# Kernel tuning notes

Hardware: AMD Instinct MI355X
Metric: run time of the kernel (lower is better)

## Reference

```python
import jax, jax.numpy as jnp
import numpy as np

N_USERS = 200000
N_ITEMS = 100000
LATENT_DIM = 32
N_INTER = 1000000  # user-item interactions; symmetric adjacency has 2*N_INTER edges


def setup_inputs() -> dict:
    key = jax.random.key(0)
    ku, ki = jax.random.split(key)
    user_emb = jax.random.normal(ku, (N_USERS, LATENT_DIM), dtype=jnp.float32) * 0.1
    item_emb = jax.random.normal(ki, (N_ITEMS, LATENT_DIM), dtype=jnp.float32) * 0.1

    # Build the symmetric normalized adjacency L = D^-0.5 A D^-0.5 in COO form,
    # mirroring get_norm_adj_mat(). Users occupy rows [0, n_users), items rows
    # [n_users, n_users+n_items).
    rng = np.random.default_rng(0)
    u = rng.integers(0, N_USERS, size=N_INTER).astype(np.int32)
    it = rng.integers(0, N_ITEMS, size=N_INTER).astype(np.int32) + N_USERS
    row = np.concatenate([u, it])   # [2*N_INTER]
    col = np.concatenate([it, u])   # [2*N_INTER]
    deg = np.bincount(row, minlength=N_USERS + N_ITEMS).astype(np.float32)
    dinv = np.power(deg + 1e-7, -0.5).astype(np.float32)
    val = dinv[row] * dinv[col]

    return {
        "user_emb": user_emb,
        "item_emb": item_emb,
        "adj_row": jnp.asarray(row, dtype=jnp.int32),
        "adj_col": jnp.asarray(col, dtype=jnp.int32),
        "adj_val": jnp.asarray(val, dtype=jnp.float32),
        "n_layers": 3,
    }


def reference(user_emb, item_emb, adj_row, adj_col, adj_val, n_layers):
    n_users = user_emb.shape[0]
    n_nodes = n_users + item_emb.shape[0]
    e = jnp.concatenate([user_emb, item_emb], axis=0)  # [N, D] ego embeddings
    acc = e
    for _ in range(n_layers):
        # SpMM: e <- L @ e via gather + segment_sum over COO edges
        msgs = adj_val[:, None] * e[adj_col]               # [nnz, D]
        e = jax.ops.segment_sum(msgs, adj_row, num_segments=n_nodes)
        acc = acc + e
    out = acc / float(n_layers + 1)  # mean over stacked layer embeddings
    return out[:n_users], out[n_users:]
```

## Files before the change

### kernel.cpp

```cpp
#include <hip/hip_runtime.h>

#define D 32
#define BSH 9
#define BRWS 512
#define EC 8192
#define NBMAX 1024

__device__ __forceinline__ unsigned short f2bf(float f) {
    unsigned u = __float_as_uint(f);
    return (unsigned short)((u + 0x7FFFu + ((u >> 16) & 1u)) >> 16);
}
__device__ __forceinline__ float bflo(unsigned v) { return __uint_as_float(v << 16); }
__device__ __forceinline__ float bfhi(unsigned v) { return __uint_as_float(v & 0xFFFF0000u); }

__global__ void zero_int_kernel(int* __restrict__ p, int n) {
    int i = blockIdx.x * blockDim.x + threadIdx.x;
    if (i < n) p[i] = 0;
}

__global__ void bhist_kernel(const int* __restrict__ row, int* __restrict__ gcnt,
                             int nnz, int nb) {
    __shared__ int h[NBMAX];
    for (int i = threadIdx.x; i < NBMAX; i += blockDim.x) h[i] = 0;
    __syncthreads();
    int stride = gridDim.x * blockDim.x;
    for (int i = blockIdx.x * blockDim.x + threadIdx.x; i < nnz; i += stride)
        atomicAdd(&h[row[i] >> BSH], 1);
    __syncthreads();
    for (int i = threadIdx.x; i < nb; i += blockDim.x)
        if (h[i]) atomicAdd(&gcnt[i], h[i]);
}

__global__ void bscan_kernel(const int* __restrict__ gcnt, int* __restrict__ gbase,
                             int* __restrict__ gcur, int nb, int nnz) {
    __shared__ int lds[256];
    int t = threadIdx.x;
    int base = t * 4;
    int v[4];
    int s = 0;
#pragma unroll
    for (int k = 0; k < 4; ++k) {
        v[k] = (base + k < nb) ? gcnt[base + k] : 0;
        s += v[k];
    }
    lds[t] = s;
    __syncthreads();
    for (int off = 1; off < 256; off <<= 1) {
        int x = lds[t];
        int y = (t >= off) ? lds[t - off] : 0;
        __syncthreads();
        lds[t] = x + y;
        __syncthreads();
    }
    int run = lds[t] - s;
#pragma unroll
    for (int k = 0; k < 4; ++k) {
        if (base + k < nb) { gbase[base + k] = run; gcur[base + k] = run; }
        run += v[k];
    }
    if (t == 0) gbase[nb] = nnz;
}

__global__ __launch_bounds__(256) void part_kernel(
    const int* __restrict__ row, const int* __restrict__ col,
    int* __restrict__ gcur, unsigned* __restrict__ be, int nnz) {
    __shared__ int h[NBMAX];
    __shared__ int cur[NBMAX];
    int c0 = blockIdx.x * EC;
    int c1 = c0 + EC;
    if (c1 > nnz) c1 = nnz;
    for (int i = threadIdx.x; i < NBMAX; i += blockDim.x) h[i] = 0;
    __syncthreads();
    for (int i = c0 + threadIdx.x; i < c1; i += blockDim.x)
        atomicAdd(&h[row[i] >> BSH], 1);
    __syncthreads();
    for (int i = threadIdx.x; i < NBMAX; i += blockDim.x) {
        int c = h[i];
        cur[i] = c ? atomicAdd(&gcur[i], c) : 0;
    }
    __syncthreads();
    for (int i = c0 + threadIdx.x; i < c1; i += blockDim.x) {
        int r = row[i];
        int pos = atomicAdd(&cur[r >> BSH], 1);
        be[pos] = ((unsigned)(r & (BRWS - 1)) << 19) | (unsigned)col[i];
    }
}

__global__ __launch_bounds__(256) void lcsr_kernel(
    const int* __restrict__ gbase, const unsigned* __restrict__ be,
    int* __restrict__ ci, int* __restrict__ ptr,
    float* __restrict__ dinv, float* __restrict__ rds,
    int n_nodes, int nnz) {
    __shared__ int cnt[BRWS];
    __shared__ int cur[BRWS];
    __shared__ int sc[256];
    int b = blockIdx.x;
    int t = threadIdx.x;
    cnt[2 * t] = 0;
    cnt[2 * t + 1] = 0;
    __syncthreads();
    int s0 = gbase[b], s1 = gbase[b + 1];
    for (int j = s0 + t; j < s1; j += 256)
        atomicAdd(&cnt[be[j] >> 19], 1);
    __syncthreads();
    int v0 = cnt[2 * t], v1 = cnt[2 * t + 1];
    int s = v0 + v1;
    sc[t] = s;
    __syncthreads();
    for (int off = 1; off < 256; off <<= 1) {
        int x = sc[t];
        int y = (t >= off) ? sc[t - off] : 0;
        __syncthreads();
        sc[t] = x + y;
        __syncthreads();
    }
    int ex = sc[t] - s;
    int gr = b * BRWS + 2 * t;
    if (gr < n_nodes) {
        ptr[gr] = s0 + ex;
        float r_ = sqrtf((float)v0 + 1e-7f);
        dinv[gr] = 1.0f / r_;
        rds[gr] = r_;
    }
    if (gr + 1 < n_nodes) {
        ptr[gr + 1] = s0 + ex + v0;
        float r_ = sqrtf((float)v1 + 1e-7f);
        dinv[gr + 1] = 1.0f / r_;
        rds[gr + 1] = r_;
    }
    cur[2 * t] = s0 + ex;
    cur[2 * t + 1] = s0 + ex + v0;
    if (b == 0 && t == 0) ptr[n_nodes] = nnz;
    __syncthreads();
    for (int j = s0 + t; j < s1; j += 256) {
        unsigned e = be[j];
        int pos = atomicAdd(&cur[e >> 19], 1);
        ci[pos] = (int)((e & 0x7FFFFu) << 5);
    }
}

__global__ void init_em_kernel(const float* __restrict__ ue, const float* __restrict__ ie,
                               const float* __restrict__ dinv,
                               uint2* __restrict__ em, int nu4, int total4) {
    int stride = gridDim.x * blockDim.x;
    for (int i = blockIdx.x * blockDim.x + threadIdx.x; i < total4; i += stride) {
        float4 v = (i < nu4) ? ((const float4*)ue)[i] : ((const float4*)ie)[i - nu4];
        float dv = dinv[i >> 3];
        uint2 w;
        w.x = (unsigned)f2bf(dv * v.x) | ((unsigned)f2bf(dv * v.y) << 16);
        w.y = (unsigned)f2bf(dv * v.z) | ((unsigned)f2bf(dv * v.w) << 16);
        em[i] = w;
    }
}

__device__ __forceinline__ void upk8(uint4 u, float* s) {
    s[0] += bflo(u.x); s[1] += bfhi(u.x);
    s[2] += bflo(u.y); s[3] += bfhi(u.y);
    s[4] += bflo(u.z); s[5] += bfhi(u.z);
    s[6] += bflo(u.w); s[7] += bfhi(u.w);
}

__global__ __launch_bounds__(256) void spmm_kernel(
    const int* __restrict__ ptr, const int* __restrict__ ci,
    const unsigned short* __restrict__ em_in, uint4* __restrict__ em_out,
    const float* __restrict__ dinv, const float* __restrict__ rds,
    const float* __restrict__ ue, const float* __restrict__ ie,
    const uint4* __restrict__ em1, const uint4* __restrict__ em2,
    float4* __restrict__ out, int n_nodes, int nu_elems, int mode) {
    int t = blockIdx.x * blockDim.x + threadIdx.x;
    int r = t >> 2;
    int lq = t & 3;
    if (r >= n_nodes) return;
    int j = ptr[r];
    int j1 = ptr[r + 1];
    float s[8] = {0.f, 0.f, 0.f, 0.f, 0.f, 0.f, 0.f, 0.f};
    const char* base = (const char*)em_in + (size_t)(lq << 4);
    for (; j + 3 < j1; j += 4) {
        int c0 = ci[j], c1 = ci[j + 1], c2 = ci[j + 2], c3 = ci[j + 3];
        uint4 a = *(const uint4*)(base + ((size_t)c0 << 1));
        uint4 b = *(const uint4*)(base + ((size_t)c1 << 1));
        uint4 c = *(const uint4*)(base + ((size_t)c2 << 1));
        uint4 e = *(const uint4*)(base + ((size_t)c3 << 1));
        upk8(a, s); upk8(b, s); upk8(c, s); upk8(e, s);
    }
    if (j + 1 < j1) {
        int c0 = ci[j], c1 = ci[j + 1];
        uint4 a = *(const uint4*)(base + ((size_t)c0 << 1));
        uint4 b = *(const uint4*)(base + ((size_t)c1 << 1));
        upk8(a, s); upk8(b, s);
        j += 2;
    }
    if (j < j1) {
        uint4 a = *(const uint4*)(base + ((size_t)ci[j] << 1));
        upk8(a, s);
    }
    float dv = dinv[r];
    int q = (r << 2) + lq;
    if (mode == 0) {
        float sc = dv * dv;
        uint4 w;
        w.x = (unsigned)f2bf(sc * s[0]) | ((unsigned)f2bf(sc * s[1]) << 16);
        w.y = (unsigned)f2bf(sc * s[2]) | ((unsigned)f2bf(sc * s[3]) << 16);
        w.z = (unsigned)f2bf(sc * s[4]) | ((unsigned)f2bf(sc * s[5]) << 16);
        w.w = (unsigned)f2bf(sc * s[6]) | ((unsigned)f2bf(sc * s[7]) << 16);
        em_out[q] = w;
    } else {
        int q4 = (r << 3) + (lq << 1);
        int nu4 = nu_elems >> 2;
        float4 e0a = (q4 < nu4) ? ((const float4*)ue)[q4] : ((const float4*)ie)[q4 - nu4];
        float4 e0b = (q4 + 1 < nu4) ? ((const float4*)ue)[q4 + 1] : ((const float4*)ie)[q4 + 1 - nu4];
        uint4 m1 = em1[q], m2 = em2[q];
        float rd = rds[r];
        float4 oa, ob;
        oa.x = 0.25f * (e0a.x + rd * (bflo(m1.x) + bflo(m2.x)) + dv * s[0]);
        oa.y = 0.25f * (e0a.y + rd * (bfhi(m1.x) + bfhi(m2.x)) + dv * s[1]);
        oa.z = 0.25f * (e0a.z + rd * (bflo(m1.y) + bflo(m2.y)) + dv * s[2]);
        oa.w = 0.25f * (e0a.w + rd * (bfhi(m1.y) + bfhi(m2.y)) + dv * s[3]);
        ob.x = 0.25f * (e0b.x + rd * (bflo(m1.z) + bflo(m2.z)) + dv * s[4]);
        ob.y = 0.25f * (e0b.y + rd * (bfhi(m1.z) + bfhi(m2.z)) + dv * s[5]);
        ob.z = 0.25f * (e0b.z + rd * (bflo(m1.w) + bflo(m2.w)) + dv * s[6]);
        ob.w = 0.25f * (e0b.w + rd * (bfhi(m1.w) + bfhi(m2.w)) + dv * s[7]);
        out[q4] = oa;
        out[q4 + 1] = ob;
    }
}

extern "C" void kernel_launch(void* const* d_in, const int* in_sizes, int n_in,
                              void* d_out, int out_size, void* d_ws, size_t ws_size,
                              hipStream_t stream) {
    const float* ue  = (const float*)d_in[0];
    const float* ie  = (const float*)d_in[1];
    const int*   row = (const int*)d_in[2];
    const int*   col = (const int*)d_in[3];

    const int nu_elems = in_sizes[0];
    const int ni_elems = in_sizes[1];
    const int nnz      = in_sizes[2];
    const int total    = nu_elems + ni_elems;
    const int n_nodes  = total / D;
    const int nb       = (n_nodes + BRWS - 1) >> BSH;

    float4* out = (float4*)d_out;

    char* ws = (char*)d_ws;
    unsigned short* em0 = (unsigned short*)ws;  ws += (size_t)total * 2;
    unsigned short* em1 = (unsigned short*)ws;  ws += (size_t)total * 2;
    unsigned short* em2 = (unsigned short*)ws;  ws += (size_t)total * 2;
    unsigned* be = (unsigned*)ws;  ws += (size_t)nnz * 4;
    int*   ci    = (int*)ws;       ws += (size_t)nnz * 4;
    int*   ptr   = (int*)ws;       ws += (size_t)(n_nodes + 2) * 4;
    float* dinv  = (float*)ws;     ws += (size_t)n_nodes * 4;
    float* rds   = (float*)ws;     ws += (size_t)n_nodes * 4;
    int*   gcnt  = (int*)ws;       ws += (size_t)NBMAX * 4;
    int*   gbase = (int*)ws;       ws += (size_t)(NBMAX + 2) * 4;
    int*   gcur  = (int*)ws;

    const int blk = 256;
    int total4 = total / 4;
    int g_init = (total4 + blk - 1) / blk;
    if (g_init > 2048) g_init = 2048;
    int g_part = (nnz + EC - 1) / EC;
    int g_spmm = (n_nodes * 4 + blk - 1) / blk;

    zero_int_kernel<<<(nb + blk - 1) / blk, blk, 0, stream>>>(gcnt, nb);
    bhist_kernel<<<120, blk, 0, stream>>>(row, gcnt, nnz, nb);
    bscan_kernel<<<1, 256, 0, stream>>>(gcnt, gbase, gcur, nb, nnz);

    part_kernel<<<g_part, blk, 0, stream>>>(row, col, gcur, be, nnz);
    lcsr_kernel<<<nb, blk, 0, stream>>>(gbase, be, ci, ptr, dinv, rds, n_nodes, nnz);

    init_em_kernel<<<g_init, blk, 0, stream>>>(ue, ie, dinv, (uint2*)em0,
                                               nu_elems / 4, total4);

    spmm_kernel<<<g_spmm, blk, 0, stream>>>(ptr, ci, em0, (uint4*)em1, dinv, rds,
                                            ue, ie, (const uint4*)em1, (const uint4*)em2,
                                            out, n_nodes, nu_elems, 0);
    spmm_kernel<<<g_spmm, blk, 0, stream>>>(ptr, ci, em1, (uint4*)em2, dinv, rds,
                                            ue, ie, (const uint4*)em1, (const uint4*)em2,
                                            out, n_nodes, nu_elems, 0);
    spmm_kernel<<<g_spmm, blk, 0, stream>>>(ptr, ci, em2, (uint4*)em2, dinv, rds,
                                            ue, ie, (const uint4*)em1, (const uint4*)em2,
                                            out, n_nodes, nu_elems, 1);
}
```

Baseline: 202.8 us.

## Fuse bucket scan into partition and CSR kernels, fold embedding init into CSR build

Drops the separate zero, scan and init_em kernels. Each part_kernel and lcsr_kernel block now recomputes the bucket-offset prefix scan locally, and lcsr_kernel writes the scaled bf16 ego embeddings for its row range. A single memset clears the counters, the partition chunk size is halved, and the histogram grid is doubled. This saves launch overhead and one pass over dinv, but every block repeats a redundant 1024-entry scan.

```diff
diff --git a/kernel.cpp b/kernel.cpp
--- a/kernel.cpp
+++ b/kernel.cpp
@@ -3,7 +3,7 @@
 #define D 32
 #define BSH 9
 #define BRWS 512
-#define EC 8192
+#define EC 4096
 #define NBMAX 1024
 
 __device__ __forceinline__ unsigned short f2bf(float f) {
@@ -12,11 +12,6 @@
 }
 __device__ __forceinline__ float bflo(unsigned v) { return __uint_as_float(v << 16); }
 __device__ __forceinline__ float bfhi(unsigned v) { return __uint_as_float(v & 0xFFFF0000u); }
-
-__global__ void zero_int_kernel(int* __restrict__ p, int n) {
-    int i = blockIdx.x * blockDim.x + threadIdx.x;
-    if (i < n) p[i] = 0;
-}
 
 __global__ void bhist_kernel(const int* __restrict__ row, int* __restrict__ gcnt,
                              int nnz, int nb) {
@@ -31,80 +26,75 @@
         if (h[i]) atomicAdd(&gcnt[i], h[i]);
 }
 
-__global__ void bscan_kernel(const int* __restrict__ gcnt, int* __restrict__ gbase,
-                             int* __restrict__ gcur, int nb, int nnz) {
-    __shared__ int lds[256];
+__global__ __launch_bounds__(256) void part_kernel(
+    const int* __restrict__ row, const int* __restrict__ col,
+    const int* __restrict__ gcnt, int* __restrict__ gcuroff,
+    unsigned* __restrict__ be, int nnz, int nb) {
+    __shared__ int h[NBMAX];
+    __shared__ int gb[NBMAX];
+    __shared__ int sc[256];
     int t = threadIdx.x;
-    int base = t * 4;
     int v[4];
     int s = 0;
 #pragma unroll
     for (int k = 0; k < 4; ++k) {
-        v[k] = (base + k < nb) ? gcnt[base + k] : 0;
+        int idx = t * 4 + k;
+        v[k] = (idx < nb) ? gcnt[idx] : 0;
         s += v[k];
-    }
-    lds[t] = s;
+        h[idx] = 0;
+    }
+    sc[t] = s;
     __syncthreads();
     for (int off = 1; off < 256; off <<= 1) {
-        int x = lds[t];
-        int y = (t >= off) ? lds[t - off] : 0;
-        __syncthreads();
-        lds[t] = x + y;
-        __syncthreads();
-    }
-    int run = lds[t] - s;
-#pragma unroll
-    for (int k = 0; k < 4; ++k) {
-        if (base + k < nb) { gbase[base + k] = run; gcur[base + k] = run; }
-        run += v[k];
-    }
-    if (t == 0) gbase[nb] = nnz;
-}
-
-__global__ __launch_bounds__(256) void part_kernel(
-    const int* __restrict__ row, const int* __restrict__ col,
-    int* __restrict__ gcur, unsigned* __restrict__ be, int nnz) {
-    __shared__ int h[NBMAX];
-    __shared__ int cur[NBMAX];
+        int x = sc[t];
+        int y = (t >= off) ? sc[t - off] : 0;
+        __syncthreads();
+        sc[t] = x + y;
+        __syncthreads();
+    }
+    int run = sc[t] - s;
+#pragma unroll
+    for (int k = 0; k < 4; ++k) { gb[t * 4 + k] = run; run += v[k]; }
+    __syncthreads();
+
     int c0 = blockIdx.x * EC;
     int c1 = c0 + EC;
     if (c1 > nnz) c1 = nnz;
-    for (int i = threadIdx.x; i < NBMAX; i += blockDim.x) h[i] = 0;
-    __syncthreads();
-    for (int i = c0 + threadIdx.x; i < c1; i += blockDim.x)
+    for (int i = c0 + t; i < c1; i += 256)
         atomicAdd(&h[row[i] >> BSH], 1);
     __syncthreads();
-    for (int i = threadIdx.x; i < NBMAX; i += blockDim.x) {
+    for (int i = t; i < NBMAX; i += 256) {
         int c = h[i];
-        cur[i] = c ? atomicAdd(&gcur[i], c) : 0;
-    }
-    __syncthreads();
-    for (int i = c0 + threadIdx.x; i < c1; i += blockDim.x) {
+        if (c) h[i] = gb[i] + atomicAdd(&gcuroff[i], c);
+    }
+    __syncthreads();
+    for (int i = c0 + t; i < c1; i += 256) {
         int r = row[i];
-        int pos = atomicAdd(&cur[r >> BSH], 1);
+        int pos = atomicAdd(&h[r >> BSH], 1);
         be[pos] = ((unsigned)(r & (BRWS - 1)) << 19) | (unsigned)col[i];
     }
 }
 
 __global__ __launch_bounds__(256) void lcsr_kernel(
-    const int* __restrict__ gbase, const unsigned* __restrict__ be,
+    const int* __restrict__ gcnt, const unsigned* __restrict__ be,
     int* __restrict__ ci, int* __restrict__ ptr,
     float* __restrict__ dinv, float* __restrict__ rds,
-    int n_nodes, int nnz) {
+    const float4* __restrict__ ue4, const float4* __restrict__ ie4,
+    uint2* __restrict__ em0, int n_nodes, int nnz, int nb, int nu4) {
+    __shared__ int gb[NBMAX];
     __shared__ int cnt[BRWS];
     __shared__ int cur[BRWS];
     __shared__ int sc[256];
     int b = blockIdx.x;
     int t = threadIdx.x;
-    cnt[2 * t] = 0;
-    cnt[2 * t + 1] = 0;
-    __syncthreads();
-    int s0 = gbase[b], s1 = gbase[b + 1];
-    for (int j = s0 + t; j < s1; j += 256)
-        atomicAdd(&cnt[be[j] >> 19], 1);
-    __syncthreads();
-    int v0 = cnt[2 * t], v1 = cnt[2 * t + 1];
-    int s = v0 + v1;
+    int v[4];
+    int s = 0;
+#pragma unroll
+    for (int k = 0; k < 4; ++k) {
+        int idx = t * 4 + k;
+        v[k] = (idx < nb) ? gcnt[idx] : 0;
+        s += v[k];
+    }
     sc[t] = s;
     __syncthreads();
     for (int off = 1; off < 256; off <<= 1) {
@@ -114,19 +104,44 @@
         sc[t] = x + y;
         __syncthreads();
     }
-    int ex = sc[t] - s;
+    int run = sc[t] - s;
+#pragma unroll
+    for (int k = 0; k < 4; ++k) { gb[t * 4 + k] = run; run += v[k]; }
+    cnt[2 * t] = 0;
+    cnt[2 * t + 1] = 0;
+    __syncthreads();
+
+    int s0 = gb[b];
+    int s1 = s0 + gcnt[b];
+    for (int j = s0 + t; j < s1; j += 256)
+        atomicAdd(&cnt[be[j] >> 19], 1);
+    __syncthreads();
+    int v0 = cnt[2 * t], v1 = cnt[2 * t + 1];
+    int sp = v0 + v1;
+    sc[t] = sp;
+    __syncthreads();
+    for (int off = 1; off < 256; off <<= 1) {
+        int x = sc[t];
+        int y = (t >= off) ? sc[t - off] : 0;
+        __syncthreads();
+        sc[t] = x + y;
+        __syncthreads();
+    }
+    int ex = sc[t] - sp;
     int gr = b * BRWS + 2 * t;
+    float r0 = sqrtf((float)v0 + 1e-7f);
+    float r1 = sqrtf((float)v1 + 1e-7f);
+    float di0 = 1.0f / r0;
+    float di1 = 1.0f / r1;
     if (gr < n_nodes) {
         ptr[gr] = s0 + ex;
-        float r_ = sqrtf((float)v0 + 1e-7f);
-        dinv[gr] = 1.0f / r_;
-        rds[gr] = r_;
+        dinv[gr] = di0;
+        rds[gr] = r0;
     }
     if (gr + 1 < n_nodes) {
         ptr[gr + 1] = s0 + ex + v0;
-        float r_ = sqrtf((float)v1 + 1e-7f);
-        dinv[gr + 1] = 1.0f / r_;
-        rds[gr + 1] = r_;
+        dinv[gr + 1] = di1;
+        rds[gr + 1] = r1;
     }
     cur[2 * t] = s0 + ex;
     cur[2 * t + 1] = s0 + ex + v0;
@@ -137,19 +152,22 @@
         int pos = atomicAdd(&cur[e >> 19], 1);
         ci[pos] = (int)((e & 0x7FFFFu) << 5);
     }
-}
-
-__global__ void init_em_kernel(const float* __restrict__ ue, const float* __restrict__ ie,
-                               const float* __restrict__ dinv,
-                               uint2* __restrict__ em, int nu4, int total4) {
-    int stride = gridDim.x * blockDim.x;
-    for (int i = blockIdx.x * blockDim.x + threadIdx.x; i < total4; i += stride) {
-        float4 v = (i < nu4) ? ((const float4*)ue)[i] : ((const float4*)ie)[i - nu4];
-        float dv = dinv[i >> 3];
+    __syncthreads();
+    cnt[2 * t] = __float_as_int(di0);
+    cnt[2 * t + 1] = __float_as_int(di1);
+    __syncthreads();
+    int base = b * BRWS;
+    int rmax = n_nodes - base;
+    if (rmax > BRWS) rmax = BRWS;
+    for (int i = t; i < rmax * 8; i += 256) {
+        int rl = i >> 3;
+        int q4 = ((base + rl) << 3) + (i & 7);
+        float4 vv = (q4 < nu4) ? ue4[q4] : ie4[q4 - nu4];
+        float dv = __int_as_float(cnt[rl]);
         uint2 w;
-        w.x = (unsigned)f2bf(dv * v.x) | ((unsigned)f2bf(dv * v.y) << 16);
-        w.y = (unsigned)f2bf(dv * v.z) | ((unsigned)f2bf(dv * v.w) << 16);
-        em[i] = w;
+        w.x = (unsigned)f2bf(dv * vv.x) | ((unsigned)f2bf(dv * vv.y) << 16);
+        w.y = (unsigned)f2bf(dv * vv.z) | ((unsigned)f2bf(dv * vv.w) << 16);
+        em0[q4] = w;
     }
 }
 
@@ -252,25 +270,19 @@
     float* dinv  = (float*)ws;     ws += (size_t)n_nodes * 4;
     float* rds   = (float*)ws;     ws += (size_t)n_nodes * 4;
     int*   gcnt  = (int*)ws;       ws += (size_t)NBMAX * 4;
-    int*   gbase = (int*)ws;       ws += (size_t)(NBMAX + 2) * 4;
-    int*   gcur  = (int*)ws;
+    int*   gcuroff = (int*)ws;
 
     const int blk = 256;
-    int total4 = total / 4;
-    int g_init = (total4 + blk - 1) / blk;
-    if (g_init > 2048) g_init = 2048;
     int g_part = (nnz + EC - 1) / EC;
     int g_spmm = (n_nodes * 4 + blk - 1) / blk;
 
-    zero_int_kernel<<<(nb + blk - 1) / blk, blk, 0, stream>>>(gcnt, nb);
-    bhist_kernel<<<120, blk, 0, stream>>>(row, gcnt, nnz, nb);
-    bscan_kernel<<<1, 256, 0, stream>>>(gcnt, gbase, gcur, nb, nnz);
-
-    part_kernel<<<g_part, blk, 0, stream>>>(row, col, gcur, be, nnz);
-    lcsr_kernel<<<nb, blk, 0, stream>>>(gbase, be, ci, ptr, dinv, rds, n_nodes, nnz);
-
-    init_em_kernel<<<g_init, blk, 0, stream>>>(ue, ie, dinv, (uint2*)em0,
-                                               nu_elems / 4, total4);
+    hipMemsetAsync(gcnt, 0, (size_t)NBMAX * 2 * 4, stream);
+
+    bhist_kernel<<<240, blk, 0, stream>>>(row, gcnt, nnz, nb);
+    part_kernel<<<g_part, blk, 0, stream>>>(row, col, gcnt, gcuroff, be, nnz, nb);
+    lcsr_kernel<<<nb, blk, 0, stream>>>(gcnt, be, ci, ptr, dinv, rds,
+                                        (const float4*)ue, (const float4*)ie,
+                                        (uint2*)em0, n_nodes, nnz, nb, nu_elems / 4);
 
     spmm_kernel<<<g_spmm, blk, 0, stream>>>(ptr, ci, em0, (uint4*)em1, dinv, rds,
                                             ue, ie, (const uint4*)em1, (const uint4*)em2,
```

Result: faster. 193.3 us (-4.7%).
